# Optimization experiments

Hardware: AMD Instinct MI355X
Metric: run time of the kernel (lower is better)

The kernel has to match this reference:

```python
import math
import jax
import jax.numpy as jnp
import numpy as np

B, L, C = 16, 512, 1024
N_HEAD = 8
HEAD = C // N_HEAD


def setup_inputs() -> dict:
    key = jax.random.key(0)
    k1, k2, k3, k4, k5, k6 = jax.random.split(key, 6)
    x = jax.random.normal(k1, (B, L, C), dtype=jnp.float32)
    # binary adjacency (0/1) as float, as in graph data
    adj = jax.random.randint(k2, (B, L, L), 0, 2).astype(jnp.float32)
    W_qkv = jax.random.normal(k3, (C, 3 * C), dtype=jnp.float32) * (1.0 / math.sqrt(C))
    b_qkv = jax.random.normal(k4, (3 * C,), dtype=jnp.float32) * 0.02
    W_d = jax.random.normal(k5, (1, C), dtype=jnp.float32)
    b_d = jax.random.normal(k6, (C,), dtype=jnp.float32) * 0.02
    return {"x": x, "adj": adj, "W_qkv": W_qkv, "b_qkv": b_qkv, "W_d": W_d, "b_d": b_d}


def reference(x, adj, W_qkv, b_qkv, W_d, b_d):
    # degree gating (self.degree == True)
    degree = adj.sum(-1, keepdims=True)                      # [B,L,1]
    gate = jax.nn.sigmoid(degree @ W_d + b_d)                # [B,L,C]
    x = x * gate
    # fused qkv projection, chunk into qk / res / value
    qkv = x @ W_qkv + b_qkv                                  # [B,L,3C]
    qk, res, value = jnp.split(qkv, 3, axis=-1)
    def heads(t):                                            # [B,L,C] -> [B,H,L,hd]
        return t.reshape(B, L, N_HEAD, HEAD).transpose(0, 2, 1, 3)
    qk, res, value = heads(qk), heads(res), heads(value)
    qk = jax.nn.sigmoid(qk)
    # sigmoid-kernel attention scores
    attn = jnp.einsum("bhld,bhmd->bhlm", qk, qk) / math.sqrt(HEAD)
    # adjacency masking (rel_pos_bias == True)
    attn = jnp.where(adj[:, None, :, :] == 0, 0.0, attn)
    # sum-normalization instead of softmax
    attn = attn / (attn.sum(-1, keepdims=True) + 1e-6)
    out = jnp.einsum("bhlm,bhmd->bhld", attn, value) + res   # residual from qkv chunk
    out = out.transpose(0, 2, 1, 3).reshape(B, L, C)
    return jax.nn.relu(out)
```

## Files before the change

### kernel.cpp

```cpp
#include <hip/hip_runtime.h>
#include <math.h>

#define BDIM 16
#define LDIM 512
#define CDIM 1024
#define NH 8
#define HD 128
#define MROWS (BDIM * LDIM)
#define N3 (3 * CDIM)

typedef unsigned short u16;
typedef unsigned long long u64;
typedef short s8v __attribute__((ext_vector_type(8)));
typedef short s4v __attribute__((ext_vector_type(4)));
typedef float f32x4 __attribute__((ext_vector_type(4)));

__device__ __forceinline__ float sigmoidf_(float z) {
    return 1.0f / (1.0f + __expf(-z));
}
__device__ __forceinline__ u16 f2bf(float f) {
    union { float f; unsigned int u; } v; v.f = f;
    unsigned int u = v.u;
    unsigned int r = (u + 0x7FFFu + ((u >> 16) & 1u)) >> 16;
    return (u16)r;
}
__device__ __forceinline__ float bf2f(u16 b) {
    union { unsigned int u; float f; } v; v.u = ((unsigned int)b) << 16;
    return v.f;
}

__global__ void degree_kernel(const float* __restrict__ adj, float* __restrict__ deg,
                              u64* __restrict__ adjbits) {
    int row = blockIdx.x;
    int lane = threadIdx.x;
    const float* a = adj + (size_t)row * LDIM;
    float s = 0.f;
    #pragma unroll
    for (int mc = 0; mc < LDIM; mc += 64) {
        float v = a[mc + lane];
        s += v;
        u64 m = __ballot(v != 0.f);
        if (lane == 0) adjbits[(size_t)row * (LDIM / 64) + (mc >> 6)] = m;
    }
    #pragma unroll
    for (int off = 32; off > 0; off >>= 1) s += __shfl_down(s, off);
    if (lane == 0) deg[row] = s;
}

__global__ void gate_kernel(const float* __restrict__ x, const float* __restrict__ deg,
                            const float* __restrict__ Wd, const float* __restrict__ bd,
                            u16* __restrict__ xg) {
    int row = blockIdx.x;
    int t = threadIdx.x;
    float d = deg[row];
    float4 xv = ((const float4*)(x + (size_t)row * CDIM))[t];
    float4 wv = ((const float4*)Wd)[t];
    float4 bv = ((const float4*)bd)[t];
    s4v o;
    o.x = (short)f2bf(xv.x * sigmoidf_(d * wv.x + bv.x));
    o.y = (short)f2bf(xv.y * sigmoidf_(d * wv.y + bv.y));
    o.z = (short)f2bf(xv.z * sigmoidf_(d * wv.z + bv.z));
    o.w = (short)f2bf(xv.w * sigmoidf_(d * wv.w + bv.w));
    ((s4v*)(xg + (size_t)row * CDIM))[t] = o;
}

__global__ void packW_kernel(const float* __restrict__ W, u16* __restrict__ Wt) {
    __shared__ float tile[64][65];
    int k0 = blockIdx.x * 64, n0 = blockIdx.y * 64;
    int tx = threadIdx.x & 63, ty = threadIdx.x >> 6;
    #pragma unroll
    for (int yy = ty; yy < 64; yy += 4)
        tile[yy][tx] = W[(size_t)(k0 + yy) * N3 + n0 + tx];
    __syncthreads();
    #pragma unroll
    for (int yy = ty; yy < 64; yy += 4)
        Wt[(size_t)(n0 + yy) * CDIM + k0 + tx] = f2bf(tile[tx][yy]);
}

__global__ __launch_bounds__(256, 3) void gemm_bf16_kernel(const u16* __restrict__ A,
                                                           const u16* __restrict__ Bt,
                                                           const float* __restrict__ bias,
                                                           u16* __restrict__ ksig,
                                                           u16* __restrict__ resb,
                                                           u16* __restrict__ vt) {
    __shared__ __align__(16) u16 As[128 * 64];
    __shared__ __align__(16) u16 Bs[128 * 64];
    int t = threadIdx.x;
    int m0 = blockIdx.y * 128, n0 = blockIdx.x * 128;
    int lane = t & 63, w = t >> 6;
    int i15 = lane & 15, quad = lane >> 4;
    int wm = w >> 1, wn = w & 1;

    f32x4 acc[4][4];
    #pragma unroll
    for (int i = 0; i < 4; ++i)
        #pragma unroll
        for (int j = 0; j < 4; ++j) acc[i][j] = (f32x4)(0.f);

    for (int k0 = 0; k0 < CDIM; k0 += 64) {
        #pragma unroll
        for (int p = 0; p < 4; ++p) {
            int sb = (w * 4 + p) * 64;
            int s = sb + lane;
            int row = s >> 3;
            int seg = (s & 7) ^ (row & 7);
            const u16* ga = A + (size_t)(m0 + row) * CDIM + k0 + seg * 8;
            const u16* gb = Bt + (size_t)(n0 + row) * CDIM + k0 + seg * 8;
            __builtin_amdgcn_global_load_lds(
                (const __attribute__((address_space(1))) unsigned int*)ga,
                (__attribute__((address_space(3))) unsigned int*)&As[sb * 8], 16, 0, 0);
            __builtin_amdgcn_global_load_lds(
                (const __attribute__((address_space(1))) unsigned int*)gb,
                (__attribute__((address_space(3))) unsigned int*)&Bs[sb * 8], 16, 0, 0);
        }
        __syncthreads();
        #pragma unroll
        for (int kc = 0; kc < 2; ++kc) {
            s8v aF[4], bF[4];
            #pragma unroll
            for (int mt = 0; mt < 4; ++mt) {
                int row = wm * 64 + mt * 16 + i15;
                int slot = row * 8 + ((kc * 4 + quad) ^ (i15 & 7));
                aF[mt] = *(const s8v*)&As[slot * 8];
            }
            #pragma unroll
            for (int nt = 0; nt < 4; ++nt) {
                int row = wn * 64 + nt * 16 + i15;
                int slot = row * 8 + ((kc * 4 + quad) ^ (i15 & 7));
                bF[nt] = *(const s8v*)&Bs[slot * 8];
            }
            #pragma unroll
            for (int mt = 0; mt < 4; ++mt)
                #pragma unroll
                for (int nt = 0; nt < 4; ++nt)
                    acc[mt][nt] = __builtin_amdgcn_mfma_f32_16x16x32_bf16(aF[mt], bF[nt], acc[mt][nt], 0, 0, 0);
        }
        __syncthreads();
    }

    int chunk = n0 >> 10;
    #pragma unroll
    for (int nt = 0; nt < 4; ++nt) {
        int ncol = n0 + wn * 64 + nt * 16 + i15;
        float bv = bias[ncol];
        #pragma unroll
        for (int mt = 0; mt < 4; ++mt) {
            int mbase = m0 + wm * 64 + mt * 16 + quad * 4;
            if (chunk == 0) {
                int h = (ncol >> 7) & 7, d = ncol & 127;
                #pragma unroll
                for (int r = 0; r < 4; ++r) {
                    int mrow = mbase + r;
                    int bb = mrow >> 9, l = mrow & 511;
                    ksig[(((size_t)bb * NH + h) * LDIM + l) * HD + d] = f2bf(sigmoidf_(acc[mt][nt][r] + bv));
                }
            } else if (chunk == 1) {
                #pragma unroll
                for (int r = 0; r < 4; ++r) {
                    int mrow = mbase + r;
                    resb[(size_t)mrow * CDIM + (ncol - CDIM)] = f2bf(acc[mt][nt][r] + bv);
                }
            } else {
                int h = (ncol >> 7) & 7, d = ncol & 127;
                int bb = mbase >> 9, l = mbase & 511;
                s4v pk;
                pk.x = (short)f2bf(acc[mt][nt][0] + bv);
                pk.y = (short)f2bf(acc[mt][nt][1] + bv);
                pk.z = (short)f2bf(acc[mt][nt][2] + bv);
                pk.w = (short)f2bf(acc[mt][nt][3] + bv);
                *(s4v*)&vt[(((size_t)bb * NH + h) * HD + d) * LDIM + l] = pk;
            }
        }
    }
}

__global__ __launch_bounds__(256) void attn_kernel(const u16* __restrict__ ksig,
                                                   const u16* __restrict__ vt,
                                                   const u16* __restrict__ resb,
                                                   const u64* __restrict__ adjbits,
                                                   float* __restrict__ out) {
    __shared__ __align__(16) u16 lds_ks[64 * 128];
    __shared__ __align__(16) u16 lds_vt[128 * 64];
    __shared__ __align__(16) u16 lds_ps[4][16][72];

    int t = threadIdx.x;
    int lane = t & 63, w = t >> 6;
    int i15 = lane & 15, quad = lane >> 4;
    int bid = blockIdx.x;
    int l0 = (bid >> 7) * 64;
    int b  = (bid >> 3) & 15;
    int h  = bid & 7;

    const u16* ksig_bh = ksig + ((size_t)b * NH + h) * LDIM * HD;
    const u16* vt_bh   = vt + ((size_t)b * NH + h) * HD * LDIM;
    const u64* abits   = adjbits + ((size_t)b * LDIM + l0 + w * 16 + quad * 4) * (LDIM / 64);

    s8v aQ[4];
    {
        const u16* qrow = ksig_bh + (size_t)(l0 + w * 16 + i15) * HD + quad * 8;
        #pragma unroll
        for (int kc = 0; kc < 4; ++kc) aQ[kc] = *(const s8v*)(qrow + kc * 32);
    }

    f32x4 accO[8];
    #pragma unroll
    for (int i = 0; i < 8; ++i) accO[i] = (f32x4)(0.f);
    float prs[4] = {0.f, 0.f, 0.f, 0.f};

    const float scale = 0.08838834764831845f;

    for (int m0 = 0; m0 < LDIM; m0 += 64) {
        #pragma unroll
        for (int p = 0; p < 4; ++p) {
            int sb = (w * 4 + p) * 64;
            int s = sb + lane;
            int row = s >> 4;
            int seg = (s & 15) ^ (row & 15);
            const u16* g = ksig_bh + (size_t)(m0 + row) * HD + seg * 8;
            __builtin_amdgcn_global_load_lds(
                (const __attribute__((address_space(1))) unsigned int*)g,
                (__attribute__((address_space(3))) unsigned int*)&lds_ks[sb * 8], 16, 0, 0);
        }
        #pragma unroll
        for (int p = 0; p < 4; ++p) {
            int sb = (w * 4 + p) * 64;
            int s = sb + lane;
            int row = s >> 3;
            int seg = (s & 7) ^ (row & 7);
            const u16* g = vt_bh + (size_t)row * LDIM + m0 + seg * 8;
            __builtin_amdgcn_global_load_lds(
                (const __attribute__((address_space(1))) unsigned int*)g,
                (__attribute__((address_space(3))) unsigned int*)&lds_vt[sb * 8], 16, 0, 0);
        }
        unsigned int mw0[4], mw1[4];
        #pragma unroll
        for (int r = 0; r < 4; ++r) {
            u64 wrd = abits[(size_t)r * (LDIM / 64) + (m0 >> 6)];
            mw0[r] = (unsigned int)wrd;
            mw1[r] = (unsigned int)(wrd >> 32);
        }
        __syncthreads();

        f32x4 S[4];
        #pragma unroll
        for (int nt = 0; nt < 4; ++nt) {
            S[nt] = (f32x4)(0.f);
            #pragma unroll
            for (int kc = 0; kc < 4; ++kc) {
                int row = nt * 16 + i15;
                int slot = row * 16 + ((kc * 4 + quad) ^ (row & 15));
                s8v bK = *(const s8v*)&lds_ks[slot * 8];
                S[nt] = __builtin_amdgcn_mfma_f32_16x16x32_bf16(aQ[kc], bK, S[nt], 0, 0, 0);
            }
        }

        #pragma unroll
        for (int nt = 0; nt < 4; ++nt) {
            int sh = (nt & 1) * 16 + i15;
            #pragma unroll
            for (int r = 0; r < 4; ++r) {
                unsigned int half = (nt < 2) ? mw0[r] : mw1[r];
                float p = ((half >> sh) & 1u) ? S[nt][r] * scale : 0.f;
                prs[r] += p;
                lds_ps[w][quad * 4 + r][nt * 16 + i15] = f2bf(p);
            }
        }

        {
            s8v aP[2];
            #pragma unroll
            for (int ks = 0; ks < 2; ++ks)
                aP[ks] = *(const s8v*)&lds_ps[w][i15][ks * 32 + quad * 8];
            #pragma unroll
            for (int ntd = 0; ntd < 8; ++ntd) {
                #pragma unroll
                for (int ks = 0; ks < 2; ++ks) {
                    int row = ntd * 16 + i15;
                    int slot = row * 8 + ((ks * 4 + quad) ^ (row & 7));
                    s8v bV = *(const s8v*)&lds_vt[slot * 8];
                    accO[ntd] = __builtin_amdgcn_mfma_f32_16x16x32_bf16(aP[ks], bV, accO[ntd], 0, 0, 0);
                }
            }
        }
        __syncthreads();
    }

    float inv[4];
    #pragma unroll
    for (int r = 0; r < 4; ++r) {
        float s = prs[r];
        s += __shfl_xor(s, 1);
        s += __shfl_xor(s, 2);
        s += __shfl_xor(s, 4);
        s += __shfl_xor(s, 8);
        inv[r] = 1.0f / (s + 1e-6f);
    }
    #pragma unroll
    for (int ntd = 0; ntd < 8; ++ntd) {
        int dcol = h * HD + ntd * 16 + i15;
        #pragma unroll
        for (int r = 0; r < 4; ++r) {
            size_t idx = ((size_t)b * LDIM + l0 + w * 16 + quad * 4 + r) * CDIM + dcol;
            float v = accO[ntd][r] * inv[r] + bf2f(resb[idx]);
            out[idx] = fmaxf(v, 0.f);
        }
    }
}

extern "C" void kernel_launch(void* const* d_in, const int* in_sizes, int n_in,
                              void* d_out, int out_size, void* d_ws, size_t ws_size,
                              hipStream_t stream) {
    (void)in_sizes; (void)n_in; (void)out_size; (void)ws_size;
    const float* x     = (const float*)d_in[0];
    const float* adj   = (const float*)d_in[1];
    const float* W_qkv = (const float*)d_in[2];
    const float* b_qkv = (const float*)d_in[3];
    const float* W_d   = (const float*)d_in[4];
    const float* b_d   = (const float*)d_in[5];
    float* out = (float*)d_out;

    char* ws = (char*)d_ws;
    size_t off = 0;
    float* deg  = (float*)(ws + off); off += 32768;
    u64* adjb   = (u64*)(ws + off);   off += (size_t)MROWS * 8 * 8;
    u16*   xg   = (u16*)(ws + off);   off += (size_t)MROWS * CDIM * 2;
    u16*   Wt   = (u16*)(ws + off);   off += (size_t)N3 * CDIM * 2;
    u16*   ksig = (u16*)(ws + off);   off += (size_t)MROWS * CDIM * 2;
    u16*   resb = (u16*)(ws + off);   off += (size_t)MROWS * CDIM * 2;
    u16*   vt   = (u16*)(ws + off);   off += (size_t)MROWS * CDIM * 2;

    degree_kernel<<<MROWS, 64, 0, stream>>>(adj, deg, adjb);
    gate_kernel<<<MROWS, 256, 0, stream>>>(x, deg, W_d, b_d, xg);
    packW_kernel<<<dim3(CDIM / 64, N3 / 64), 256, 0, stream>>>(W_qkv, Wt);
    gemm_bf16_kernel<<<dim3(N3 / 128, MROWS / 128), 256, 0, stream>>>(xg, Wt, b_qkv, ksig, resb, vt);
    attn_kernel<<<LDIM / 64 * NH * BDIM, 256, 0, stream>>>(ksig, vt, resb, adjb, out);
}
```

Measured before the change: 210.9 us.

## Fuse degree and gate kernels; double attention query tile per block

Merges the degree/adjacency-bitmask kernel into the gating kernel, so the degree array and one launch are no longer needed. The attention kernel now processes 128 query rows per block (32 per wave, as two 16-row MFMA tiles), so each K/V tile staged in LDS is reused across twice as many rows. This halves global K/V traffic and the block count in exchange for more accumulator registers per wave and possibly lower occupancy.

```diff
diff --git a/kernel.cpp b/kernel.cpp
--- a/kernel.cpp
+++ b/kernel.cpp
@@ -29,30 +29,32 @@
     return v.f;
 }
 
-__global__ void degree_kernel(const float* __restrict__ adj, float* __restrict__ deg,
-                              u64* __restrict__ adjbits) {
-    int row = blockIdx.x;
-    int lane = threadIdx.x;
-    const float* a = adj + (size_t)row * LDIM;
-    float s = 0.f;
-    #pragma unroll
-    for (int mc = 0; mc < LDIM; mc += 64) {
-        float v = a[mc + lane];
-        s += v;
-        u64 m = __ballot(v != 0.f);
-        if (lane == 0) adjbits[(size_t)row * (LDIM / 64) + (mc >> 6)] = m;
-    }
-    #pragma unroll
-    for (int off = 32; off > 0; off >>= 1) s += __shfl_down(s, off);
-    if (lane == 0) deg[row] = s;
-}
-
-__global__ void gate_kernel(const float* __restrict__ x, const float* __restrict__ deg,
-                            const float* __restrict__ Wd, const float* __restrict__ bd,
-                            u16* __restrict__ xg) {
+__global__ __launch_bounds__(256) void deg_gate_kernel(const float* __restrict__ adj,
+                                                       const float* __restrict__ x,
+                                                       const float* __restrict__ Wd,
+                                                       const float* __restrict__ bd,
+                                                       u16* __restrict__ xg,
+                                                       u64* __restrict__ adjbits) {
+    __shared__ float wsum[4];
     int row = blockIdx.x;
     int t = threadIdx.x;
-    float d = deg[row];
+    int w = t >> 6, lane = t & 63;
+    const float* a = adj + (size_t)row * LDIM;
+    float v0 = a[w * 128 + lane];
+    float v1 = a[w * 128 + 64 + lane];
+    u64 b0 = __ballot(v0 != 0.f);
+    u64 b1 = __ballot(v1 != 0.f);
+    if (lane == 0) {
+        adjbits[(size_t)row * (LDIM / 64) + 2 * w]     = b0;
+        adjbits[(size_t)row * (LDIM / 64) + 2 * w + 1] = b1;
+    }
+    float s = v0 + v1;
+    #pragma unroll
+    for (int off = 32; off > 0; off >>= 1) s += __shfl_down(s, off);
+    if (lane == 0) wsum[w] = s;
+    __syncthreads();
+    float d = wsum[0] + wsum[1] + wsum[2] + wsum[3];
+
     float4 xv = ((const float4*)(x + (size_t)row * CDIM))[t];
     float4 wv = ((const float4*)Wd)[t];
     float4 bv = ((const float4*)bd)[t];
@@ -181,31 +183,35 @@
                                                    float* __restrict__ out) {
     __shared__ __align__(16) u16 lds_ks[64 * 128];
     __shared__ __align__(16) u16 lds_vt[128 * 64];
-    __shared__ __align__(16) u16 lds_ps[4][16][72];
+    __shared__ __align__(16) u16 lds_ps[4][32][72];
 
     int t = threadIdx.x;
     int lane = t & 63, w = t >> 6;
     int i15 = lane & 15, quad = lane >> 4;
     int bid = blockIdx.x;
-    int l0 = (bid >> 7) * 64;
+    int l0 = (bid >> 7) * 128;
     int b  = (bid >> 3) & 15;
     int h  = bid & 7;
+    int lw = l0 + w * 32;
 
     const u16* ksig_bh = ksig + ((size_t)b * NH + h) * LDIM * HD;
     const u16* vt_bh   = vt + ((size_t)b * NH + h) * HD * LDIM;
-    const u64* abits   = adjbits + ((size_t)b * LDIM + l0 + w * 16 + quad * 4) * (LDIM / 64);
-
-    s8v aQ[4];
-    {
-        const u16* qrow = ksig_bh + (size_t)(l0 + w * 16 + i15) * HD + quad * 8;
-        #pragma unroll
-        for (int kc = 0; kc < 4; ++kc) aQ[kc] = *(const s8v*)(qrow + kc * 32);
-    }
-
-    f32x4 accO[8];
-    #pragma unroll
-    for (int i = 0; i < 8; ++i) accO[i] = (f32x4)(0.f);
-    float prs[4] = {0.f, 0.f, 0.f, 0.f};
+    const u64* abits   = adjbits + ((size_t)b * LDIM) * (LDIM / 64);
+
+    s8v aQ[2][4];
+    #pragma unroll
+    for (int mt = 0; mt < 2; ++mt) {
+        const u16* qrow = ksig_bh + (size_t)(lw + mt * 16 + i15) * HD + quad * 8;
+        #pragma unroll
+        for (int kc = 0; kc < 4; ++kc) aQ[mt][kc] = *(const s8v*)(qrow + kc * 32);
+    }
+
+    f32x4 accO[2][8];
+    #pragma unroll
+    for (int mt = 0; mt < 2; ++mt)
+        #pragma unroll
+        for (int i = 0; i < 8; ++i) accO[mt][i] = (f32x4)(0.f);
+    float prs[2][4] = {{0.f, 0.f, 0.f, 0.f}, {0.f, 0.f, 0.f, 0.f}};
 
     const float scale = 0.08838834764831845f;
 
@@ -232,45 +238,57 @@
                 (const __attribute__((address_space(1))) unsigned int*)g,
                 (__attribute__((address_space(3))) unsigned int*)&lds_vt[sb * 8], 16, 0, 0);
         }
-        unsigned int mw0[4], mw1[4];
-        #pragma unroll
-        for (int r = 0; r < 4; ++r) {
-            u64 wrd = abits[(size_t)r * (LDIM / 64) + (m0 >> 6)];
-            mw0[r] = (unsigned int)wrd;
-            mw1[r] = (unsigned int)(wrd >> 32);
-        }
+        unsigned int mw0[2][4], mw1[2][4];
+        #pragma unroll
+        for (int mt = 0; mt < 2; ++mt)
+            #pragma unroll
+            for (int r = 0; r < 4; ++r) {
+                u64 wrd = abits[(size_t)(lw + mt * 16 + quad * 4 + r) * (LDIM / 64) + (m0 >> 6)];
+                mw0[mt][r] = (unsigned int)wrd;
+                mw1[mt][r] = (unsigned int)(wrd >> 32);
+            }
         __syncthreads();
 
-        f32x4 S[4];
+        f32x4 S[2][4];
+        #pragma unroll
+        for (int mt = 0; mt < 2; ++mt)
+            #pragma unroll
+            for (int nt = 0; nt < 4; ++nt) S[mt][nt] = (f32x4)(0.f);
         #pragma unroll
         for (int nt = 0; nt < 4; ++nt) {
-            S[nt] = (f32x4)(0.f);
             #pragma unroll
             for (int kc = 0; kc < 4; ++kc) {
                 int row = nt * 16 + i15;
                 int slot = row * 16 + ((kc * 4 + quad) ^ (row & 15));
                 s8v bK = *(const s8v*)&lds_ks[slot * 8];
-                S[nt] = __builtin_amdgcn_mfma_f32_16x16x32_bf16(aQ[kc], bK, S[nt], 0, 0, 0);
-            }
-        }
-
-        #pragma unroll
-        for (int nt = 0; nt < 4; ++nt) {
-            int sh = (nt & 1) * 16 + i15;
-            #pragma unroll
-            for (int r = 0; r < 4; ++r) {
-                unsigned int half = (nt < 2) ? mw0[r] : mw1[r];
-                float p = ((half >> sh) & 1u) ? S[nt][r] * scale : 0.f;
-                prs[r] += p;
-                lds_ps[w][quad * 4 + r][nt * 16 + i15] = f2bf(p);
+                #pragma unroll
+                for (int mt = 0; mt < 2; ++mt)
+                    S[mt][nt] = __builtin_amdgcn_mfma_f32_16x16x32_bf16(aQ[mt][kc], bK, S[mt][nt], 0, 0, 0);
+            }
+        }
+
+        #pragma unroll
+        for (int mt = 0; mt < 2; ++mt) {
+            #pragma unroll
+            for (int nt = 0; nt < 4; ++nt) {
+                int sh = (nt & 1) * 16 + i15;
+                #pragma unroll
+                for (int r = 0; r < 4; ++r) {
+                    unsigned int half = (nt < 2) ? mw0[mt][r] : mw1[mt][r];
+                    float p = ((half >> sh) & 1u) ? S[mt][nt][r] * scale : 0.f;
+                    prs[mt][r] += p;
+                    lds_ps[w][mt * 16 + quad * 4 + r][nt * 16 + i15] = f2bf(p);
+                }
             }
         }
 
         {
-            s8v aP[2];
-            #pragma unroll
-            for (int ks = 0; ks < 2; ++ks)
-                aP[ks] = *(const s8v*)&lds_ps[w][i15][ks * 32 + quad * 8];
+            s8v aP[2][2];
+            #pragma unroll
+            for (int mt = 0; mt < 2; ++mt)
+                #pragma unroll
+                for (int ks = 0; ks < 2; ++ks)
+                    aP[mt][ks] = *(const s8v*)&lds_ps[w][mt * 16 + i15][ks * 32 + quad * 8];
             #pragma unroll
             for (int ntd = 0; ntd < 8; ++ntd) {
                 #pragma unroll
@@ -278,31 +296,36 @@
                     int row = ntd * 16 + i15;
                     int slot = row * 8 + ((ks * 4 + quad) ^ (row & 7));
                     s8v bV = *(const s8v*)&lds_vt[slot * 8];
-                    accO[ntd] = __builtin_amdgcn_mfma_f32_16x16x32_bf16(aP[ks], bV, accO[ntd], 0, 0, 0);
+                    #pragma unroll
+                    for (int mt = 0; mt < 2; ++mt)
+                        accO[mt][ntd] = __builtin_amdgcn_mfma_f32_16x16x32_bf16(aP[mt][ks], bV, accO[mt][ntd], 0, 0, 0);
                 }
             }
         }
         __syncthreads();
     }
 
-    float inv[4];
-    #pragma unroll
-    for (int r = 0; r < 4; ++r) {
-        float s = prs[r];
-        s += __shfl_xor(s, 1);
-        s += __shfl_xor(s, 2);
-        s += __shfl_xor(s, 4);
-        s += __shfl_xor(s, 8);
-        inv[r] = 1.0f / (s + 1e-6f);
-    }
-    #pragma unroll
-    for (int ntd = 0; ntd < 8; ++ntd) {
-        int dcol = h * HD + ntd * 16 + i15;
+    #pragma unroll
+    for (int mt = 0; mt < 2; ++mt) {
+        float inv[4];
         #pragma unroll
         for (int r = 0; r < 4; ++r) {
-            size_t idx = ((size_t)b * LDIM + l0 + w * 16 + quad * 4 + r) * CDIM + dcol;
-            float v = accO[ntd][r] * inv[r] + bf2f(resb[idx]);
-            out[idx] = fmaxf(v, 0.f);
+            float s = prs[mt][r];
+            s += __shfl_xor(s, 1);
+            s += __shfl_xor(s, 2);
+            s += __shfl_xor(s, 4);
+            s += __shfl_xor(s, 8);
+            inv[r] = 1.0f / (s + 1e-6f);
+        }
+        #pragma unroll
+        for (int ntd = 0; ntd < 8; ++ntd) {
+            int dcol = h * HD + ntd * 16 + i15;
+            #pragma unroll
+            for (int r = 0; r < 4; ++r) {
+                size_t idx = ((size_t)b * LDIM + lw + mt * 16 + quad * 4 + r) * CDIM + dcol;
+                float v = accO[mt][ntd][r] * inv[r] + bf2f(resb[idx]);
+                out[idx] = fmaxf(v, 0.f);
+            }
         }
     }
 }
@@ -321,7 +344,6 @@
 
     char* ws = (char*)d_ws;
     size_t off = 0;
-    float* deg  = (float*)(ws + off); off += 32768;
     u64* adjb   = (u64*)(ws + off);   off += (size_t)MROWS * 8 * 8;
     u16*   xg   = (u16*)(ws + off);   off += (size_t)MROWS * CDIM * 2;
     u16*   Wt   = (u16*)(ws + off);   off += (size_t)N3 * CDIM * 2;
@@ -329,9 +351,8 @@
     u16*   resb = (u16*)(ws + off);   off += (size_t)MROWS * CDIM * 2;
     u16*   vt   = (u16*)(ws + off);   off += (size_t)MROWS * CDIM * 2;
 
-    degree_kernel<<<MROWS, 64, 0, stream>>>(adj, deg, adjb);
-    gate_kernel<<<MROWS, 256, 0, stream>>>(x, deg, W_d, b_d, xg);
+    deg_gate_kernel<<<MROWS, 256, 0, stream>>>(adj, x, W_d, b_d, xg, adjb);
     packW_kernel<<<dim3(CDIM / 64, N3 / 64), 256, 0, stream>>>(W_qkv, Wt);
     gemm_bf16_kernel<<<dim3(N3 / 128, MROWS / 128), 256, 0, stream>>>(xg, Wt, b_qkv, ksig, resb, vt);
-    attn_kernel<<<LDIM / 64 * NH * BDIM, 256, 0, stream>>>(ksig, vt, resb, adjb, out);
-}
+    attn_kernel<<<LDIM / 128 * NH * BDIM, 256, 0, stream>>>(ksig, vt, resb, adjb, out);
+}
```

New measurement: 218.4 us. 1.04x slower.
